# Performance work log

Measured on AMD Instinct MI355X. Metric: run time of the kernel, lower is better.

The kernel has to match this reference:

```python
import jax, jax.numpy as jnp
import numpy as np

NUM_EMBEDDINGS = 8192
EMBEDDING_DIM = 256
COMMITMENT_COST = 0.25


def setup_inputs() -> dict:
    key = jax.random.key(0)
    k1, k2 = jax.random.split(key)
    x = jax.random.normal(k1, (8, 4096, EMBEDDING_DIM), dtype=jnp.float32)
    # torch init: uniform(-1/K, 1/K)
    codebook = jax.random.uniform(
        k2, (NUM_EMBEDDINGS, EMBEDDING_DIM), dtype=jnp.float32,
        minval=-1.0 / NUM_EMBEDDINGS, maxval=1.0 / NUM_EMBEDDINGS)
    return {"x": x, "codebook": codebook}


def reference(x, codebook):
    D = codebook.shape[1]
    K = codebook.shape[0]
    flat_x = x.reshape(-1, D)                      # [N, D]
    distances = (jnp.sum(flat_x * flat_x, axis=1, keepdims=True)
                 + jnp.sum(codebook * codebook, axis=1)
                 - 2.0 * jnp.matmul(flat_x, codebook.T))
    encoding_indices = jnp.argmin(distances, axis=1)  # [N]
    # direct gather instead of one-hot matmul (same math)
    quantized = codebook[encoding_indices].reshape(x.shape)

    sg = jax.lax.stop_gradient
    e_latent_loss = jnp.mean((sg(quantized) - x) ** 2)
    q_latent_loss = jnp.mean((quantized - sg(x)) ** 2)
    loss = q_latent_loss + COMMITMENT_COST * e_latent_loss

    quantized_st = x + sg(quantized - x)

    # avg one-hot probs via counts
    counts = jnp.bincount(encoding_indices, length=K)
    avg_probs = counts.astype(x.dtype) / encoding_indices.shape[0]
    perplexity = jnp.exp(-jnp.sum(avg_probs * jnp.log(avg_probs + 1e-10)))
    return quantized_st, loss, perplexity
```

## Files before the change

kernel.cpp:

```cpp
#include <hip/hip_runtime.h>
#include <cfloat>
#include <math.h>

#define NUM_EMB 8192
#define DIM 256
#define NROWS 32768
#define NSPLIT 4
#define CHUNKS 32

typedef float f32x4 __attribute__((ext_vector_type(4)));
typedef float f32x2 __attribute__((ext_vector_type(2)));
typedef int   i32x4 __attribute__((ext_vector_type(4)));
typedef int   i32x8 __attribute__((ext_vector_type(8)));

#define GL2LDS(g, l) __builtin_amdgcn_global_load_lds( \
    (const __attribute__((address_space(1))) void*)(g), \
    (__attribute__((address_space(3))) void*)(l), 16, 0, 0)
#define GL2LDS4(g, l) __builtin_amdgcn_global_load_lds( \
    (const __attribute__((address_space(1))) void*)(g), \
    (__attribute__((address_space(3))) void*)(l), 4, 0, 0)

#define MFMA(A, B, C) __builtin_amdgcn_mfma_scale_f32_16x16x128_f8f6f4( \
    (A), (B), (C), 0, 0, 0, 127, 0, 127)

#define DSR(dst, addr, IMM) \
    asm volatile("ds_read_b128 %0, %1 offset:%2" : "=v"(dst) : "v"(addr), "n"(IMM))
#define DSR2(dst, addr, O0, O1) \
    asm volatile("ds_read2_b32 %0, %1 offset0:%2 offset1:%3" \
                 : "=v"(dst) : "v"(addr), "n"(O0), "n"(O1))

__global__ __launch_bounds__(256) void vq_prep(const float* __restrict__ x,
                                               unsigned char* __restrict__ xq,
                                               const float* __restrict__ cb,
                                               unsigned char* __restrict__ cbq,
                                               float* __restrict__ cbn,
                                               unsigned int* __restrict__ counts) {
    int b = blockIdx.x;
    if (b < 2048) {
        #pragma unroll
        for (int j = 0; j < 2; j++) {
            int i = b * 512 + j * 256 + threadIdx.x;
            float4 v0 = ((const float4*)x)[2 * i];
            float4 v1 = ((const float4*)x)[2 * i + 1];
            int p0 = __builtin_amdgcn_cvt_pk_fp8_f32(-v0.x, -v0.y, 0, false);
            p0     = __builtin_amdgcn_cvt_pk_fp8_f32(-v0.z, -v0.w, p0, true);
            int p1 = __builtin_amdgcn_cvt_pk_fp8_f32(-v1.x, -v1.y, 0, false);
            p1     = __builtin_amdgcn_cvt_pk_fp8_f32(-v1.z, -v1.w, p1, true);
            ((int2*)xq)[i] = make_int2(p0, p1);
        }
    } else if (b < 4096) {
        int row  = (b - 2048) * 4 + (threadIdx.x >> 6);
        int lane = threadIdx.x & 63;
        float4 v = ((const float4*)(cb + (size_t)row * DIM))[lane];
        int p = __builtin_amdgcn_cvt_pk_fp8_f32(v.x * 8192.f, v.y * 8192.f, 0, false);
        p     = __builtin_amdgcn_cvt_pk_fp8_f32(v.z * 8192.f, v.w * 8192.f, p, true);
        ((int*)cbq)[row * 64 + lane] = p;
        float s = v.x * v.x + v.y * v.y + v.z * v.z + v.w * v.w;
        #pragma unroll
        for (int off = 32; off > 0; off >>= 1) s += __shfl_down(s, off, 64);
        if (lane == 0) cbn[row] = 4096.f * s + 256.f;
    } else {
        counts[(b - 4096) * 256 + threadIdx.x] = 0u;
    }
}

__global__ __launch_bounds__(256, 4) void vq_argmin_mfma(
        const unsigned char* __restrict__ xq,
        const unsigned char* __restrict__ cbq,
        const float* __restrict__ cbn,
        unsigned long long* __restrict__ partial) {
    __shared__ __align__(16) unsigned char Bs[2][16384];
    __shared__ __align__(16) float bnL[2][64];
    __shared__ unsigned long long redk[2][64];

    const int tid = threadIdx.x;
    const int lane = tid & 63;
    const int w = tid >> 6;
    const int wm = w >> 1, wn = w & 1;
    const int l15 = lane & 15, q = lane >> 4;
    const int ns = blockIdx.x & (NSPLIT - 1);
    const int by = blockIdx.x >> 2;
    const int m0 = by * 64;
    const int nbase = ns * (NUM_EMB / NSPLIT);

    i32x8 afr00, afr01, afr10, afr11;
    {
        const unsigned char* p = xq + (size_t)(m0 + wm * 32 + l15) * 256 + q * 32;
        i32x4 lo, hi;
        lo = *(const i32x4*)(p);                  hi = *(const i32x4*)(p + 16);
        afr00 = __builtin_shufflevector(lo, hi, 0, 1, 2, 3, 4, 5, 6, 7);
        lo = *(const i32x4*)(p + 16 * 256);       hi = *(const i32x4*)(p + 16 * 256 + 16);
        afr01 = __builtin_shufflevector(lo, hi, 0, 1, 2, 3, 4, 5, 6, 7);
        lo = *(const i32x4*)(p + 128);            hi = *(const i32x4*)(p + 128 + 16);
        afr10 = __builtin_shufflevector(lo, hi, 0, 1, 2, 3, 4, 5, 6, 7);
        lo = *(const i32x4*)(p + 16 * 256 + 128); hi = *(const i32x4*)(p + 16 * 256 + 128 + 16);
        afr11 = __builtin_shufflevector(lo, hi, 0, 1, 2, 3, 4, 5, 6, 7);
    }

    const int row0 = wn * 32 + l15;
    const int sw = row0 & 7;
    const int vA = row0 * 256 + (((2 * q) ^ sw) * 16);
    const int vB = row0 * 256 + (((2 * q + 1) ^ sw) * 16);
    const unsigned lbase =
        (unsigned)(size_t)(__attribute__((address_space(3))) void*)(void*)&Bs[0][0];
    const unsigned lbn =
        (unsigned)(size_t)(__attribute__((address_space(3))) void*)(void*)&bnL[0][0];
    const int addrA = (int)(lbase + (unsigned)vA);
    const int addrB = (int)(lbase + (unsigned)vB);

    const unsigned int colb0 = (unsigned)(wn * 32 + l15);
    const unsigned int colb1 = colb0 + 16;
    const int addrBN = (int)(lbn + 4u * colb0);

    unsigned int runk[2][4];
    #pragma unroll
    for (int i = 0; i < 2; i++)
        #pragma unroll
        for (int r = 0; r < 4; r++) runk[i][r] = 0xFFFFFFFFu;

    const int sr = lane >> 4;
    const int sv = lane & 15;
    const int kcs = sv >> 3, blk = sv & 7;
    const unsigned char* gs[4];
    int sg[4];
    #pragma unroll
    for (int t = 0; t < 4; t++) {
        int s = t * 4 + w;
        int r = s * 4 + sr;
        gs[t] = cbq + (size_t)(nbase + r) * 256 + (size_t)(kcs * 128 + ((blk ^ (r & 7)) * 16));
        sg[t] = s * 1024;
    }
    const float* bnq = cbn + nbase + lane;

    GL2LDS4(bnq, (char*)&bnL[0][0]);
    #pragma unroll
    for (int t = 0; t < 4; t++) GL2LDS(gs[t], (char*)&Bs[0][0] + sg[t]);
    #pragma unroll
    for (int t = 0; t < 4; t++) gs[t] += 16384;
    bnq += 64;

#define CHUNK_BODY(CHV, CUR, NXT, LAST) do { \
    if (!(LAST)) { \
        GL2LDS4(bnq, (char*)&bnL[NXT][0]); \
        GL2LDS(gs[0], (char*)&Bs[NXT][0] + sg[0]); \
        GL2LDS(gs[1], (char*)&Bs[NXT][0] + sg[1]); \
        GL2LDS(gs[2], (char*)&Bs[NXT][0] + sg[2]); \
        GL2LDS(gs[3], (char*)&Bs[NXT][0] + sg[3]); \
        asm volatile("s_waitcnt vmcnt(5)" ::: "memory"); \
    } else { \
        asm volatile("s_waitcnt vmcnt(0)" ::: "memory"); \
    } \
    __builtin_amdgcn_sched_barrier(0); \
    __builtin_amdgcn_s_barrier(); \
    gs[0] += 16384; gs[1] += 16384; gs[2] += 16384; gs[3] += 16384; \
    bnq += 64; \
    f32x2 bn2; \
    DSR2(bn2, addrBN, (CUR) * 64, (CUR) * 64 + 16); \
    i32x4 b0l, b0h, b1l, b1h, b2l, b2h, b3l, b3h; \
    DSR(b0l, addrA, (CUR) * 16384 + 0); \
    DSR(b0h, addrB, (CUR) * 16384 + 0); \
    DSR(b2l, addrA, (CUR) * 16384 + 4096); \
    DSR(b2h, addrB, (CUR) * 16384 + 4096); \
    DSR(b1l, addrA, (CUR) * 16384 + 128); \
    DSR(b1h, addrB, (CUR) * 16384 + 128); \
    DSR(b3l, addrA, (CUR) * 16384 + 4224); \
    DSR(b3h, addrB, (CUR) * 16384 + 4224); \
    asm volatile("s_waitcnt lgkmcnt(4)" ::: "memory"); \
    __builtin_amdgcn_sched_barrier(0); \
    f32x4 ci0; ci0[0] = bn2[0]; ci0[1] = bn2[0]; ci0[2] = bn2[0]; ci0[3] = bn2[0]; \
    f32x4 ci1; ci1[0] = bn2[1]; ci1[1] = bn2[1]; ci1[2] = bn2[1]; ci1[3] = bn2[1]; \
    i32x8 b0 = __builtin_shufflevector(b0l, b0h, 0, 1, 2, 3, 4, 5, 6, 7); \
    i32x8 b2 = __builtin_shufflevector(b2l, b2h, 0, 1, 2, 3, 4, 5, 6, 7); \
    f32x4 a00 = MFMA(afr00, b0, ci0); \
    f32x4 a10 = MFMA(afr01, b0, ci0); \
    f32x4 a01 = MFMA(afr00, b2, ci1); \
    f32x4 a11 = MFMA(afr01, b2, ci1); \
    asm volatile("s_waitcnt lgkmcnt(0)" ::: "memory"); \
    __builtin_amdgcn_sched_barrier(0); \
    i32x8 b1 = __builtin_shufflevector(b1l, b1h, 0, 1, 2, 3, 4, 5, 6, 7); \
    i32x8 b3 = __builtin_shufflevector(b3l, b3h, 0, 1, 2, 3, 4, 5, 6, 7); \
    a00 = MFMA(afr10, b1, a00); \
    a10 = MFMA(afr11, b1, a10); \
    a01 = MFMA(afr10, b3, a01); \
    a11 = MFMA(afr11, b3, a11); \
    unsigned int chb = ((unsigned)(CHV)) << 6; \
    unsigned int cj0 = chb | colb0, cj1 = chb | colb1; \
    _Pragma("unroll") \
    for (int r = 0; r < 4; r++) { \
        unsigned int k00 = (__float_as_uint(a00[r]) & 0xFFFFF800u) | cj0; \
        unsigned int k01 = (__float_as_uint(a01[r]) & 0xFFFFF800u) | cj1; \
        runk[0][r] = min(min(k00, k01), runk[0][r]); \
        unsigned int k10 = (__float_as_uint(a10[r]) & 0xFFFFF800u) | cj0; \
        unsigned int k11 = (__float_as_uint(a11[r]) & 0xFFFFF800u) | cj1; \
        runk[1][r] = min(min(k10, k11), runk[1][r]); \
    } \
    __builtin_amdgcn_s_barrier(); \
} while (0)

    #pragma unroll 1
    for (int ch = 0; ch < CHUNKS; ch += 2) {
        CHUNK_BODY(ch,     0, 1, false);
        CHUNK_BODY(ch + 1, 1, 0, (ch + 1) == CHUNKS - 1);
    }

    #pragma unroll
    for (int i = 0; i < 2; i++) {
        #pragma unroll
        for (int r = 0; r < 4; r++) {
            unsigned int rk = runk[i][r];
            unsigned int gcol = (unsigned)nbase + (rk & 0x7FFu);
            unsigned long long key =
                ((unsigned long long)(rk & 0xFFFFF800u) << 32) | gcol;
            #pragma unroll
            for (int off = 8; off >= 1; off >>= 1) {
                unsigned long long o = __shfl_xor(key, off, 16);
                if (o < key) key = o;
            }
            if (l15 == 0) redk[wn][wm * 32 + i * 16 + q * 4 + r] = key;
        }
    }
    __syncthreads();
    if (tid < 64) {
        unsigned long long k0 = redk[0][tid], k1 = redk[1][tid];
        partial[(size_t)ns * NROWS + m0 + tid] = k0 < k1 ? k0 : k1;
    }
}

__global__ __launch_bounds__(256) void vq_out(const float* __restrict__ x,
                                              const float* __restrict__ cb,
                                              const unsigned long long* __restrict__ partial,
                                              float* __restrict__ out,
                                              unsigned int* __restrict__ counts,
                                              double* __restrict__ loss_part) {
    __shared__ float wred[4];
    int wv   = threadIdx.x >> 6;
    int lane = threadIdx.x & 63;
    float wsum = 0.f;
    #pragma unroll
    for (int rr = 0; rr < 4; rr++) {
        int row = blockIdx.x * 16 + wv * 4 + rr;
        unsigned long long k = 0xFFFFFFFFFFFFFFFFull;
        #pragma unroll
        for (int t = 0; t < NSPLIT; t++) {
            unsigned long long v = partial[(size_t)t * NROWS + row];
            if (v < k) k = v;
        }
        int id = (int)(unsigned int)(k & 0xffffffffu);
        float4 qv = ((const float4*)(cb + (size_t)id * DIM))[lane];
        float4 xv = ((const float4*)(x + (size_t)row * DIM))[lane];
        float dx = qv.x - xv.x, dy = qv.y - xv.y, dz = qv.z - xv.z, dw = qv.w - xv.w;
        float4 o;
        o.x = xv.x + dx; o.y = xv.y + dy; o.z = xv.z + dz; o.w = xv.w + dw;
        ((float4*)(out + (size_t)row * DIM))[lane] = o;
        float s = dx * dx + dy * dy + dz * dz + dw * dw;
        #pragma unroll
        for (int o2 = 32; o2 > 0; o2 >>= 1) s += __shfl_down(s, o2, 64);
        if (lane == 0) {
            wsum += s;
            atomicAdd(&counts[id], 1u);
        }
    }
    if (lane == 0) wred[wv] = wsum;
    __syncthreads();
    if (threadIdx.x == 0) {
        loss_part[blockIdx.x] =
            (double)wred[0] + (double)wred[1] + (double)wred[2] + (double)wred[3];
    }
}

__global__ __launch_bounds__(256) void vq_fin(const unsigned int* __restrict__ counts,
                                              const double* __restrict__ loss_part,
                                              float* __restrict__ out_tail) {
    __shared__ double sh[256];
    __shared__ double sl[256];
    int tid = threadIdx.x;
    double h = 0.0;
    for (int k = tid; k < NUM_EMB; k += 256) {
        float p = (float)counts[k] * (1.0f / 32768.0f);
        h += (double)(p * __logf(p + 1e-10f));
    }
    double ls = 0.0;
    for (int b = tid; b < NROWS / 16; b += 256) ls += loss_part[b];
    sh[tid] = h;
    sl[tid] = ls;
    __syncthreads();
    for (int o = 128; o > 0; o >>= 1) {
        if (tid < o) { sh[tid] += sh[tid + o]; sl[tid] += sl[tid + o]; }
        __syncthreads();
    }
    if (tid == 0) {
        double mean = sl[0] / (double)((size_t)NROWS * DIM);
        out_tail[0] = (float)(1.25 * mean);
        out_tail[1] = (float)exp(-sh[0]);
    }
}

extern "C" void kernel_launch(void* const* d_in, const int* in_sizes, int n_in,
                              void* d_out, int out_size, void* d_ws, size_t ws_size,
                              hipStream_t stream) {
    const float* x  = (const float*)d_in[0];
    const float* cb = (const float*)d_in[1];
    char* ws = (char*)d_ws;
    unsigned int* counts   = (unsigned int*)(ws + 256);
    float* cbn             = (float*)(ws + 33024);
    unsigned char* xq      = (unsigned char*)(ws + 65792);
    unsigned char* cbq     = (unsigned char*)(ws + 65792 + 8388608);
    unsigned long long* pp = (unsigned long long*)(ws + 65792 + 8388608 + 2097152);
    double* loss_part      = (double*)(ws + 65792 + 8388608 + 2097152 + 16777216);
    float* out = (float*)d_out;

    vq_prep       <<<4128, 256, 0, stream>>>(x, xq, cb, cbq, cbn, counts);
    vq_argmin_mfma<<<512 * NSPLIT, 256, 0, stream>>>(xq, cbq, cbn, pp);
    vq_out        <<<2048, 256, 0, stream>>>(x, cb, pp, out, counts, loss_part);
    vq_fin        <<<1, 256, 0, stream>>>(counts, loss_part, out + (size_t)NROWS * DIM);
}
```

Measured before the change: 190.8 us.

## Double waves per argmin block, each wave owning a 16-column slice of chunk

The argmin GEMM block grows from 4 to 8 waves (2x4 layout), and each wave now computes a 32x16 tile per chunk instead of 32x32. The codebook LDS staging is spread across 8 waves with two loads each, and the final cross-wave reduction covers four column groups. The goal is more latency hiding and occupancy per CU, at the cost of fewer MFMAs per LDS read, duplicated A fragments in registers, and extra barrier participants.

```diff
diff --git a/kernel.cpp b/kernel.cpp
--- a/kernel.cpp
+++ b/kernel.cpp
@@ -9,7 +9,6 @@
 #define CHUNKS 32
 
 typedef float f32x4 __attribute__((ext_vector_type(4)));
-typedef float f32x2 __attribute__((ext_vector_type(2)));
 typedef int   i32x4 __attribute__((ext_vector_type(4)));
 typedef int   i32x8 __attribute__((ext_vector_type(8)));
 
@@ -25,9 +24,8 @@
 
 #define DSR(dst, addr, IMM) \
     asm volatile("ds_read_b128 %0, %1 offset:%2" : "=v"(dst) : "v"(addr), "n"(IMM))
-#define DSR2(dst, addr, O0, O1) \
-    asm volatile("ds_read2_b32 %0, %1 offset0:%2 offset1:%3" \
-                 : "=v"(dst) : "v"(addr), "n"(O0), "n"(O1))
+#define DSR32(dst, addr, IMM) \
+    asm volatile("ds_read_b32 %0, %1 offset:%2" : "=v"(dst) : "v"(addr), "n"(IMM))
 
 __global__ __launch_bounds__(256) void vq_prep(const float* __restrict__ x,
                                                unsigned char* __restrict__ xq,
@@ -64,19 +62,19 @@
     }
 }
 
-__global__ __launch_bounds__(256, 4) void vq_argmin_mfma(
+__global__ __launch_bounds__(512, 4) void vq_argmin_mfma(
         const unsigned char* __restrict__ xq,
         const unsigned char* __restrict__ cbq,
         const float* __restrict__ cbn,
         unsigned long long* __restrict__ partial) {
     __shared__ __align__(16) unsigned char Bs[2][16384];
     __shared__ __align__(16) float bnL[2][64];
-    __shared__ unsigned long long redk[2][64];
+    __shared__ unsigned long long redk[4][64];
 
     const int tid = threadIdx.x;
     const int lane = tid & 63;
     const int w = tid >> 6;
-    const int wm = w >> 1, wn = w & 1;
+    const int wm = w >> 2, wn = w & 3;
     const int l15 = lane & 15, q = lane >> 4;
     const int ns = blockIdx.x & (NSPLIT - 1);
     const int by = blockIdx.x >> 2;
@@ -97,20 +95,18 @@
         afr11 = __builtin_shufflevector(lo, hi, 0, 1, 2, 3, 4, 5, 6, 7);
     }
 
-    const int row0 = wn * 32 + l15;
-    const int sw = row0 & 7;
+    const int row0 = wn * 16 + l15;
+    const int sw = l15 & 7;
     const int vA = row0 * 256 + (((2 * q) ^ sw) * 16);
-    const int vB = row0 * 256 + (((2 * q + 1) ^ sw) * 16);
     const unsigned lbase =
         (unsigned)(size_t)(__attribute__((address_space(3))) void*)(void*)&Bs[0][0];
     const unsigned lbn =
         (unsigned)(size_t)(__attribute__((address_space(3))) void*)(void*)&bnL[0][0];
     const int addrA = (int)(lbase + (unsigned)vA);
-    const int addrB = (int)(lbase + (unsigned)vB);
-
-    const unsigned int colb0 = (unsigned)(wn * 32 + l15);
-    const unsigned int colb1 = colb0 + 16;
-    const int addrBN = (int)(lbn + 4u * colb0);
+    const int addrB = addrA ^ 16;
+
+    const unsigned int colb = (unsigned)(wn * 16 + l15);
+    const int addrBN = (int)(lbn + 4u * colb);
 
     unsigned int runk[2][4];
     #pragma unroll
@@ -121,78 +117,56 @@
     const int sr = lane >> 4;
     const int sv = lane & 15;
     const int kcs = sv >> 3, blk = sv & 7;
-    const unsigned char* gs[4];
-    int sg[4];
-    #pragma unroll
-    for (int t = 0; t < 4; t++) {
-        int s = t * 4 + w;
-        int r = s * 4 + sr;
-        gs[t] = cbq + (size_t)(nbase + r) * 256 + (size_t)(kcs * 128 + ((blk ^ (r & 7)) * 16));
-        sg[t] = s * 1024;
-    }
+    const int rs = w * 4 + sr;
+    const unsigned char* gs =
+        cbq + (size_t)(nbase + rs) * 256 + (size_t)(kcs * 128 + ((blk ^ (rs & 7)) * 16));
+    const int sg = w * 1024;
     const float* bnq = cbn + nbase + lane;
 
     GL2LDS4(bnq, (char*)&bnL[0][0]);
-    #pragma unroll
-    for (int t = 0; t < 4; t++) GL2LDS(gs[t], (char*)&Bs[0][0] + sg[t]);
-    #pragma unroll
-    for (int t = 0; t < 4; t++) gs[t] += 16384;
+    GL2LDS(gs,        (char*)&Bs[0][0] + sg);
+    GL2LDS(gs + 8192, (char*)&Bs[0][0] + sg + 8192);
+    gs += 16384;
     bnq += 64;
 
 #define CHUNK_BODY(CHV, CUR, NXT, LAST) do { \
     if (!(LAST)) { \
         GL2LDS4(bnq, (char*)&bnL[NXT][0]); \
-        GL2LDS(gs[0], (char*)&Bs[NXT][0] + sg[0]); \
-        GL2LDS(gs[1], (char*)&Bs[NXT][0] + sg[1]); \
-        GL2LDS(gs[2], (char*)&Bs[NXT][0] + sg[2]); \
-        GL2LDS(gs[3], (char*)&Bs[NXT][0] + sg[3]); \
-        asm volatile("s_waitcnt vmcnt(5)" ::: "memory"); \
+        GL2LDS(gs,        (char*)&Bs[NXT][0] + sg); \
+        GL2LDS(gs + 8192, (char*)&Bs[NXT][0] + sg + 8192); \
+        asm volatile("s_waitcnt vmcnt(3)" ::: "memory"); \
     } else { \
         asm volatile("s_waitcnt vmcnt(0)" ::: "memory"); \
     } \
     __builtin_amdgcn_sched_barrier(0); \
     __builtin_amdgcn_s_barrier(); \
-    gs[0] += 16384; gs[1] += 16384; gs[2] += 16384; gs[3] += 16384; \
+    gs += 16384; \
     bnq += 64; \
-    f32x2 bn2; \
-    DSR2(bn2, addrBN, (CUR) * 64, (CUR) * 64 + 16); \
-    i32x4 b0l, b0h, b1l, b1h, b2l, b2h, b3l, b3h; \
-    DSR(b0l, addrA, (CUR) * 16384 + 0); \
-    DSR(b0h, addrB, (CUR) * 16384 + 0); \
-    DSR(b2l, addrA, (CUR) * 16384 + 4096); \
-    DSR(b2h, addrB, (CUR) * 16384 + 4096); \
-    DSR(b1l, addrA, (CUR) * 16384 + 128); \
-    DSR(b1h, addrB, (CUR) * 16384 + 128); \
-    DSR(b3l, addrA, (CUR) * 16384 + 4224); \
-    DSR(b3h, addrB, (CUR) * 16384 + 4224); \
-    asm volatile("s_waitcnt lgkmcnt(4)" ::: "memory"); \
-    __builtin_amdgcn_sched_barrier(0); \
-    f32x4 ci0; ci0[0] = bn2[0]; ci0[1] = bn2[0]; ci0[2] = bn2[0]; ci0[3] = bn2[0]; \
-    f32x4 ci1; ci1[0] = bn2[1]; ci1[1] = bn2[1]; ci1[2] = bn2[1]; ci1[3] = bn2[1]; \
-    i32x8 b0 = __builtin_shufflevector(b0l, b0h, 0, 1, 2, 3, 4, 5, 6, 7); \
-    i32x8 b2 = __builtin_shufflevector(b2l, b2h, 0, 1, 2, 3, 4, 5, 6, 7); \
-    f32x4 a00 = MFMA(afr00, b0, ci0); \
-    f32x4 a10 = MFMA(afr01, b0, ci0); \
-    f32x4 a01 = MFMA(afr00, b2, ci1); \
-    f32x4 a11 = MFMA(afr01, b2, ci1); \
+    float bnv; \
+    i32x4 bl, bh; \
+    DSR32(bnv, addrBN, (CUR) * 256); \
+    DSR(bl, addrA, (CUR) * 16384 + 0); \
+    DSR(bh, addrB, (CUR) * 16384 + 0); \
     asm volatile("s_waitcnt lgkmcnt(0)" ::: "memory"); \
     __builtin_amdgcn_sched_barrier(0); \
-    i32x8 b1 = __builtin_shufflevector(b1l, b1h, 0, 1, 2, 3, 4, 5, 6, 7); \
-    i32x8 b3 = __builtin_shufflevector(b3l, b3h, 0, 1, 2, 3, 4, 5, 6, 7); \
-    a00 = MFMA(afr10, b1, a00); \
-    a10 = MFMA(afr11, b1, a10); \
-    a01 = MFMA(afr10, b3, a01); \
-    a11 = MFMA(afr11, b3, a11); \
-    unsigned int chb = ((unsigned)(CHV)) << 6; \
-    unsigned int cj0 = chb | colb0, cj1 = chb | colb1; \
+    f32x4 ci; ci[0] = bnv; ci[1] = bnv; ci[2] = bnv; ci[3] = bnv; \
+    i32x8 b0 = __builtin_shufflevector(bl, bh, 0, 1, 2, 3, 4, 5, 6, 7); \
+    f32x4 a0 = MFMA(afr00, b0, ci); \
+    f32x4 a1 = MFMA(afr01, b0, ci); \
+    DSR(bl, addrA, (CUR) * 16384 + 128); \
+    DSR(bh, addrB, (CUR) * 16384 + 128); \
+    asm volatile("s_waitcnt lgkmcnt(0)" ::: "memory"); \
+    __builtin_amdgcn_sched_barrier(0); \
+    i32x8 b1 = __builtin_shufflevector(bl, bh, 0, 1, 2, 3, 4, 5, 6, 7); \
+    a0 = MFMA(afr10, b1, a0); \
+    a1 = MFMA(afr11, b1, a1); \
+    unsigned int cj = (((unsigned)(CHV)) << 6) | colb; \
     _Pragma("unroll") \
     for (int r = 0; r < 4; r++) { \
-        unsigned int k00 = (__float_as_uint(a00[r]) & 0xFFFFF800u) | cj0; \
-        unsigned int k01 = (__float_as_uint(a01[r]) & 0xFFFFF800u) | cj1; \
-        runk[0][r] = min(min(k00, k01), runk[0][r]); \
-        unsigned int k10 = (__float_as_uint(a10[r]) & 0xFFFFF800u) | cj0; \
-        unsigned int k11 = (__float_as_uint(a11[r]) & 0xFFFFF800u) | cj1; \
-        runk[1][r] = min(min(k10, k11), runk[1][r]); \
+        unsigned int k0 = (__float_as_uint(a0[r]) & 0xFFFFF800u) | cj; \
+        unsigned int k1 = (__float_as_uint(a1[r]) & 0xFFFFF800u) | cj; \
+        runk[0][r] = min(runk[0][r], k0); \
+        runk[1][r] = min(runk[1][r], k1); \
     } \
     __builtin_amdgcn_s_barrier(); \
 } while (0)
@@ -222,7 +196,10 @@
     __syncthreads();
     if (tid < 64) {
         unsigned long long k0 = redk[0][tid], k1 = redk[1][tid];
-        partial[(size_t)ns * NROWS + m0 + tid] = k0 < k1 ? k0 : k1;
+        unsigned long long k2 = redk[2][tid], k3 = redk[3][tid];
+        k0 = k0 < k1 ? k0 : k1;
+        k2 = k2 < k3 ? k2 : k3;
+        partial[(size_t)ns * NROWS + m0 + tid] = k0 < k2 ? k0 : k2;
     }
 }
 
@@ -310,7 +287,7 @@
     float* out = (float*)d_out;
 
     vq_prep       <<<4128, 256, 0, stream>>>(x, xq, cb, cbq, cbn, counts);
-    vq_argmin_mfma<<<512 * NSPLIT, 256, 0, stream>>>(xq, cbq, cbn, pp);
+    vq_argmin_mfma<<<512 * NSPLIT, 512, 0, stream>>>(xq, cbq, cbn, pp);
     vq_out        <<<2048, 256, 0, stream>>>(x, cb, pp, out, counts, loss_part);
     vq_fin        <<<1, 256, 0, stream>>>(counts, loss_part, out + (size_t)NROWS * DIM);
 }
```

New measurement: 210.9 us. 1.11x slower.
